# Kernel optimization log

Hardware: AMD Instinct MI355X
Metric: run time of the kernel (lower is better)

The kernel has to match this reference:

```python
import jax, jax.numpy as jnp
import numpy as np

N = 50000      # nodes
E = 800000     # edges (before self loops)
B = 64         # graphs in batch
D_IN, D_HID, D_LAT, N_CLS = 3, 128, 64, 2


def _gat_params(key, d_in, d_out, scale=0.1):
    k1, k2, k3 = jax.random.split(key, 3)
    return (jax.random.normal(k1, (d_in, d_out), jnp.float32) * scale,
            jax.random.normal(k2, (d_out,), jnp.float32) * scale,
            jax.random.normal(k3, (d_out,), jnp.float32) * scale,
            jnp.zeros((d_out,), jnp.float32))


def setup_inputs() -> dict:
    key = jax.random.key(0)
    ks = jax.random.split(key, 10)
    x = jax.random.normal(ks[0], (N, D_IN), jnp.float32)
    edge_index = jax.random.randint(ks[1], (2, E), 0, N, dtype=jnp.int64)
    batch = jnp.sort(jax.random.randint(ks[2], (N,), 0, B, dtype=jnp.int64))
    W1, a1s, a1d, b1 = _gat_params(ks[3], D_IN, D_HID)
    W2, a2s, a2d, b2 = _gat_params(ks[4], D_HID, D_LAT)
    W3, a3s, a3d, b3 = _gat_params(ks[5], D_LAT, D_HID)
    W4, a4s, a4d, b4 = _gat_params(ks[6], D_HID, D_IN)
    kc1, kc2 = jax.random.split(ks[7])
    Wc1 = jax.random.normal(kc1, (D_LAT, D_LAT // 2), jnp.float32) * 0.1
    bc1 = jnp.zeros((D_LAT // 2,), jnp.float32)
    Wc2 = jax.random.normal(kc2, (D_LAT // 2, N_CLS), jnp.float32) * 0.1
    bc2 = jnp.zeros((N_CLS,), jnp.float32)
    return dict(x=x, edge_index=edge_index, batch=batch,
                W1=W1, a1s=a1s, a1d=a1d, b1=b1,
                W2=W2, a2s=a2s, a2d=a2d, b2=b2,
                W3=W3, a3s=a3s, a3d=a3d, b3=b3,
                W4=W4, a4s=a4s, a4d=a4d, b4=b4,
                Wc1=Wc1, bc1=bc1, Wc2=Wc2, bc2=bc2)


def gat_conv(x, W, a_src, a_dst, bias, send, recv, n):
    # Single-head PyG GATConv: h = xW; e_ij = LeakyReLU(a_src.h_j + a_dst.h_i);
    # alpha = softmax over incoming edges of i; out_i = sum_j alpha_ij h_j + b
    h = x @ W                                   # [n, d_out]
    e = jax.nn.leaky_relu(jnp.take(h @ a_src, send) + jnp.take(h @ a_dst, recv), 0.2)
    m = jax.ops.segment_max(e, recv, num_segments=n)   # stable softmax per dst
    e = jnp.exp(e - m[recv])
    s = jax.ops.segment_sum(e, recv, num_segments=n)
    alpha = e / s[recv]                         # [E+N]
    out = jax.ops.segment_sum(alpha[:, None] * h[send], recv, num_segments=n)
    return out + bias


def reference(x, edge_index, batch,
              W1, a1s, a1d, b1, W2, a2s, a2d, b2,
              W3, a3s, a3d, b3, W4, a4s, a4d, b4,
              Wc1, bc1, Wc2, bc2):
    loop = jnp.arange(N, dtype=edge_index.dtype)
    send = jnp.concatenate([edge_index[0], loop])   # add_self_loops=True
    recv = jnp.concatenate([edge_index[1], loop])
    # encode (dropout inactive in eval)
    h = jax.nn.relu(gat_conv(x, W1, a1s, a1d, b1, send, recv, N))
    latent = gat_conv(h, W2, a2s, a2d, b2, send, recv, N)
    # decode
    h = jax.nn.relu(gat_conv(latent, W3, a3s, a3d, b3, send, recv, N))
    reconstructed = gat_conv(h, W4, a4s, a4d, b4, send, recv, N)
    # per-graph mean pooling (segment mean, replaces Python loop)
    cnt = jax.ops.segment_sum(jnp.ones((N,), latent.dtype), batch, num_segments=B)
    pooled = jax.ops.segment_sum(latent, batch, num_segments=B) / jnp.maximum(cnt, 1.0)[:, None]
    z = jax.nn.relu(pooled @ Wc1 + bc1)
    noise_pred = z @ Wc2 + bc2
    return reconstructed, latent, noise_pred
```

## Files before the change

kernel.cpp:

```cpp
#include <hip/hip_runtime.h>
#include <hip/hip_bf16.h>

typedef __hip_bfloat16 bf16;

#define N_NODES 50000
#define N_EDGES 800000
#define NB 64

#define NBUCK 256
#define BUCK_R ((N_NODES + NBUCK - 1) / NBUCK)
#define BUCK_CAP 4352
#define OVF_CAP 65536
#define NBLK1 256
#define CHUNK1 ((N_EDGES + NBLK1 - 1) / NBLK1)
#define NIT ((CHUNK1 + 255) / 256)

#define XN_BLKS ((N_NODES + 255) / 256)
#define PREP_BLKS (XN_BLKS + 20 + 1)

#define P_W1 0
#define P_A1S 384
#define P_A1D 512
#define P_B1 640
#define P_W2 768
#define P_A2S 8960
#define P_A2D 9024
#define P_B2 9088
#define P_W3 9152
#define P_A3S 17344
#define P_A3D 17472
#define P_B3 17600
#define P_W4 17728
#define P_A4S 18112
#define P_A4D 18115
#define P_B4 18118
#define P_WC1 18121
#define P_BC1 20169
#define P_WC2 20201
#define P_BC2 20265
#define P_W3S 20280
#define P_W3D 20344
#define P_TOTAL 20408

__device__ __forceinline__ float wave_sum(float v) {
#pragma unroll
    for (int o = 32; o >= 1; o >>= 1) v += __shfl_xor(v, o, 64);
    return v;
}

__device__ __forceinline__ unsigned int pk2(float a, float b) {
    bf16 x = __float2bfloat16(a);
    bf16 y = __float2bfloat16(b);
    unsigned short ux = *reinterpret_cast<unsigned short*>(&x);
    unsigned short uy = *reinterpret_cast<unsigned short*>(&y);
    return ((unsigned int)uy << 16) | ux;
}
__device__ __forceinline__ float bf_lo(unsigned int u) {
    unsigned int v = u << 16;
    return *reinterpret_cast<float*>(&v);
}
__device__ __forceinline__ float bf_hi(unsigned int u) {
    unsigned int v = u & 0xffff0000u;
    return *reinterpret_cast<float*>(&v);
}

__device__ __forceinline__ int ld_idx(const void* p, long long i, int is64) {
    return is64 ? (int)((const long long*)p)[i] : ((const int*)p)[i];
}
__device__ __forceinline__ float ldf(const void* p, int i, int isbf) {
    return isbf ? __bfloat162float(((const bf16*)p)[i]) : ((const float*)p)[i];
}
__device__ __forceinline__ void st_out(void* p, long long i, float v, int isbf) {
    if (isbf) ((bf16*)p)[i] = __float2bfloat16(v);
    else ((float*)p)[i] = v;
}

__device__ __forceinline__ float attn_p(float esv, float edi) {
    float v = esv + edi;
    float e = (v >= 0.f) ? v : 0.2f * v;
    return __expf(fminf(e, 60.f));
}

struct PTab {
    const void* src[20];
    int off[20];
    int n[20];
};

__global__ __launch_bounds__(256) void k_prep(
        const void* __restrict__ x, const void* __restrict__ eidx,
        const void* __restrict__ rW1, const void* __restrict__ rA1s,
        const void* __restrict__ rA1d, const void* __restrict__ rW3,
        const void* __restrict__ rA3s, const void* __restrict__ rA3d,
        PTab tab, float* __restrict__ pblock, float* __restrict__ x4,
        float* __restrict__ es, float* __restrict__ ed,
        int* __restrict__ gcur, int* __restrict__ ovf_cnt, int* __restrict__ flags) {
    __shared__ int scnt[2];
    __shared__ float sw[6];
    const int t = threadIdx.x;
    if (t < 2) scnt[t] = 0;
    __syncthreads();
    {
        const unsigned short* xr = (const unsigned short*)x;
        unsigned int hb = (xr[2 * t] >> 8) & 0x7F;
        if (hb >= 58 && hb <= 65) atomicAdd(&scnt[0], 1);
        if (t < 64) {
            const unsigned int* er = (const unsigned int*)eidx;
            if (er[2 * t + 1] == 0u) atomicAdd(&scnt[1], 1);
        }
    }
    __syncthreads();
    const int isbf = (scnt[0] >= 200) ? 1 : 0;
    const int is64 = (scnt[1] >= 60) ? 1 : 0;

    const int b = blockIdx.x;
    if (b < XN_BLKS) {
        if (t < 6) {
            int row = (t < 3) ? t : t - 3;
            const void* av = (t < 3) ? rA1s : rA1d;
            float s = 0.f;
            for (int k = 0; k < 128; k++)
                s = fmaf(ldf(rW1, row * 128 + k, isbf), ldf(av, k, isbf), s);
            sw[t] = s;
        }
        __syncthreads();
        int node = b * 256 + t;
        if (node < N_NODES) {
            float x0 = ldf(x, node * 3 + 0, isbf);
            float x1 = ldf(x, node * 3 + 1, isbf);
            float x2 = ldf(x, node * 3 + 2, isbf);
            float4 v = {x0, x1, x2, 0.f};
            *(float4*)&x4[node * 4] = v;
            es[node] = x0 * sw[0] + x1 * sw[1] + x2 * sw[2];
            ed[node] = x0 * sw[3] + x1 * sw[4] + x2 * sw[5];
        }
    } else if (b < XN_BLKS + 20) {
        int p = b - XN_BLKS;
        const void* s = tab.src[p];
        float* d = pblock + tab.off[p];
        int n = tab.n[p];
        for (int i = t; i < n; i += 256) d[i] = ldf(s, i, isbf);
    } else {
        if (t < NBUCK) gcur[t] = 0;
        if (t == 0) { *ovf_cnt = 0; flags[0] = isbf; flags[1] = is64; }
        if (t >= 64 && t < 128) {
            int k = t - 64;
            float s = 0.f, d = 0.f;
            for (int c = 0; c < 128; c++) {
                float wv = ldf(rW3, k * 128 + c, isbf);
                s = fmaf(wv, ldf(rA3s, c, isbf), s);
                d = fmaf(wv, ldf(rA3d, c, isbf), d);
            }
            pblock[P_W3S + k] = s;
            pblock[P_W3D + k] = d;
        }
    }
}

__global__ __launch_bounds__(256) void k_bucket(
        const void* __restrict__ eidx, const int* __restrict__ flags,
        int* __restrict__ gcur, unsigned int* __restrict__ stage,
        int* __restrict__ ovf_cnt, uint2* __restrict__ ovf) {
    __shared__ int hist[NBUCK];
    __shared__ int base[NBUCK];
    const int t = threadIdx.x;
    const int is64 = flags[1];
    const int e0 = blockIdx.x * CHUNK1;
    const int e1 = min(e0 + CHUNK1, N_EDGES);

    unsigned int ent[NIT];
    int bk[NIT];
    hist[t] = 0;
    __syncthreads();
#pragma unroll
    for (int it = 0; it < NIT; it++) {
        int e = e0 + t + it * 256;
        int b = -1;
        unsigned int en = 0;
        if (e < e1) {
            int r = ld_idx(eidx, (long long)N_EDGES + e, is64);
            int s = ld_idx(eidx, e, is64);
            b = r / BUCK_R;
            en = ((unsigned)(r - b * BUCK_R) << 16) | (unsigned)s;
            atomicAdd(&hist[b], 1);
        }
        ent[it] = en;
        bk[it] = b;
    }
    __syncthreads();
    int cnt = hist[t];
    base[t] = (cnt > 0) ? atomicAdd(&gcur[t], cnt) : 0;
    __syncthreads();
    hist[t] = 0;
    __syncthreads();
#pragma unroll
    for (int it = 0; it < NIT; it++) {
        int b = bk[it];
        if (b >= 0) {
            int l = atomicAdd(&hist[b], 1);
            int slot = base[b] + l;
            if (slot < BUCK_CAP) {
                stage[(size_t)b * BUCK_CAP + slot] = ent[it];
            } else {
                int oi = atomicAdd(ovf_cnt, 1);
                int r = b * BUCK_R + (int)(ent[it] >> 16);
                if (oi < OVF_CAP) ovf[oi] = make_uint2(ent[it] & 0xffffu, (unsigned)r);
            }
        }
    }
}

__global__ __launch_bounds__(256) void k_count2(
        const int* __restrict__ gcur, const unsigned int* __restrict__ stage,
        const int* __restrict__ ovf_cnt, const uint2* __restrict__ ovf,
        int* __restrict__ loff, int* __restrict__ bsum) {
    __shared__ int hist[256];
    __shared__ int ss[256];
    const int b = blockIdx.x;
    const int r0 = b * BUCK_R;
    const int nr = min(BUCK_R, N_NODES - r0);
    const int t = threadIdx.x;
    hist[t] = 0;
    __syncthreads();
    const int cnt = min(gcur[b], BUCK_CAP);
    const unsigned int* sb = stage + (size_t)b * BUCK_CAP;
    for (int i = t; i < cnt; i += 256) atomicAdd(&hist[sb[i] >> 16], 1);
    int oc = min(*ovf_cnt, OVF_CAP);
    for (int i = t; i < oc; i += 256) {
        int r = (int)ovf[i].y;
        if (r >= r0 && r < r0 + nr) atomicAdd(&hist[r - r0], 1);
    }
    __syncthreads();
    int v = (t < nr) ? hist[t] + 1 : 0;
    ss[t] = v;
    __syncthreads();
#pragma unroll
    for (int o = 1; o < 256; o <<= 1) {
        int add = (t >= o) ? ss[t - o] : 0;
        __syncthreads();
        ss[t] += add;
        __syncthreads();
    }
    if (t < nr) loff[r0 + t] = ss[t] - v;
    if (t == 255) bsum[b] = ss[255];
}

__global__ __launch_bounds__(256) void k_fill3(
        const int* __restrict__ gcur, const unsigned int* __restrict__ stage,
        const int* __restrict__ ovf_cnt, const uint2* __restrict__ ovf,
        const int* __restrict__ loff, const int* __restrict__ bsum,
        int* __restrict__ off, int* __restrict__ csr_send) {
    __shared__ int sbs[NBUCK];
    __shared__ int ss[NBUCK];
    __shared__ int sstart[BUCK_R];
    __shared__ int lcur[BUCK_R];
    const int b = blockIdx.x;
    const int t = threadIdx.x;
    int v = bsum[t];
    sbs[t] = v;
    ss[t] = v;
    __syncthreads();
#pragma unroll
    for (int o = 1; o < NBUCK; o <<= 1) {
        int add = (t >= o) ? ss[t - o] : 0;
        __syncthreads();
        ss[t] += add;
        __syncthreads();
    }
    const int bb = ss[b] - sbs[b];
    if (b == NBUCK - 1 && t == 0) off[N_NODES] = ss[NBUCK - 1];

    const int r0 = b * BUCK_R;
    const int nr = min(BUCK_R, N_NODES - r0);
    for (int i = t; i < nr; i += 256) {
        int st = bb + loff[r0 + i];
        sstart[i] = st;
        off[r0 + i] = st;
        lcur[i] = 1;
        csr_send[st] = r0 + i;
    }
    __syncthreads();
    const int cnt = min(gcur[b], BUCK_CAP);
    const unsigned int* sb = stage + (size_t)b * BUCK_CAP;
    for (int i = t; i < cnt; i += 256) {
        unsigned int e = sb[i];
        int rl = (int)(e >> 16);
        int l = atomicAdd(&lcur[rl], 1);
        csr_send[sstart[rl] + l] = (int)(e & 0xffffu);
    }
    int oc = min(*ovf_cnt, OVF_CAP);
    for (int i = t; i < oc; i += 256) {
        uint2 pr = ovf[i];
        int r = (int)pr.y;
        if (r >= r0 && r < r0 + nr) {
            int rl = r - r0;
            int l = atomicAdd(&lcur[rl], 1);
            csr_send[sstart[rl] + l] = (int)pr.x;
        }
    }
}

__global__ __launch_bounds__(256) void k_wsumx3(
        const float* __restrict__ x4, const float* __restrict__ es,
        const float* __restrict__ ed, const float* __restrict__ pb,
        const int* __restrict__ off, const int* __restrict__ csr_send,
        float* __restrict__ out) {
    int wid = threadIdx.x >> 6, lane = threadIdx.x & 63;
    int node = blockIdx.x * 4 + wid;
    if (node >= N_NODES) return;
    int start = off[node], end = off[node + 1];
    float edi = ed[node];
    float a0 = 0.f, a1 = 0.f, a2 = 0.f, sl = 0.f;
    for (int j = start + lane; j < end; j += 64) {
        int s = csr_send[j];
        float p = attn_p(es[s], edi);
        sl += p;
        float4 xv = *(const float4*)&x4[s * 4];
        a0 = fmaf(p, xv.x, a0);
        a1 = fmaf(p, xv.y, a1);
        a2 = fmaf(p, xv.z, a2);
    }
    float S = wave_sum(sl);
    a0 = wave_sum(a0);
    a1 = wave_sum(a1);
    a2 = wave_sum(a2);
    float inv = 1.f / S;
    a0 *= inv; a1 *= inv; a2 *= inv;
    const float* W1 = pb + P_W1;
    const float* b1 = pb + P_B1;
    int c0 = lane, c1 = lane + 64;
    float v0 = fmaf(a0, W1[c0], fmaf(a1, W1[128 + c0], fmaf(a2, W1[256 + c0], b1[c0])));
    float v1 = fmaf(a0, W1[c1], fmaf(a1, W1[128 + c1], fmaf(a2, W1[256 + c1], b1[c1])));
    out[(size_t)node * 128 + c0] = fmaxf(v0, 0.f);
    out[(size_t)node * 128 + c1] = fmaxf(v1, 0.f);
}

template <int DIN, int DINS, int DOUT, int MODE>
__global__ __launch_bounds__(256) void k_gemm(
        const float* __restrict__ in, const float* __restrict__ W,
        const float* __restrict__ as_, const float* __restrict__ ad_,
        const float* __restrict__ bias, void* __restrict__ hout,
        float* __restrict__ es, float* __restrict__ ed) {
    constexpr int KC = (DIN < 32) ? DIN : 32;
    constexpr int NCH = DIN / KC;
    constexpr int CG = DOUT / 8;
    constexpr int NT = (256 / CG) * 4;
    constexpr int NTP = NT + 4;

    __shared__ float sX[KC][NTP];
    __shared__ float sW[KC][DOUT];

    const int t = threadIdx.x;
    const int node0 = blockIdx.x * NT;
    const int nvalid = min(NT, N_NODES - node0);

    const int cg = t & (CG - 1);
    const int ng = t / CG;

    float acc[4][8] = {};

    for (int ch = 0; ch < NCH; ch++) {
        const int k0 = ch * KC;
        if (ch > 0) __syncthreads();
        for (int i = t; i < nvalid * KC; i += 256) {
            int n = i / KC, k = i - n * KC;
            sX[k][n] = in[(size_t)(node0 + n) * DINS + k0 + k];
        }
        for (int i = t; i < KC * DOUT; i += 256) {
            int k = i / DOUT, c = i - k * DOUT;
            sW[k][c] = W[(size_t)(k0 + k) * DOUT + c];
        }
        __syncthreads();

#pragma unroll 4
        for (int k = 0; k < KC; k++) {
            float4 xv = *(const float4*)&sX[k][ng * 4];
            float4 w0 = *(const float4*)&sW[k][cg * 8];
            float4 w1 = *(const float4*)&sW[k][cg * 8 + 4];
            float xs[4] = {xv.x, xv.y, xv.z, xv.w};
            float ws[8] = {w0.x, w0.y, w0.z, w0.w, w1.x, w1.y, w1.z, w1.w};
#pragma unroll
            for (int j = 0; j < 4; j++)
#pragma unroll
                for (int c = 0; c < 8; c++)
                    acc[j][c] = fmaf(xs[j], ws[c], acc[j][c]);
        }
    }

    if constexpr (MODE == 0) {
        float asv[8], adv[8];
#pragma unroll
        for (int c = 0; c < 8; c++) {
            asv[c] = as_[cg * 8 + c];
            adv[c] = ad_[cg * 8 + c];
        }
#pragma unroll
        for (int j = 0; j < 4; j++) {
            int n = ng * 4 + j;
            float e_s = 0.f, e_d = 0.f;
#pragma unroll
            for (int c = 0; c < 8; c++) {
                e_s = fmaf(acc[j][c], asv[c], e_s);
                e_d = fmaf(acc[j][c], adv[c], e_d);
            }
#pragma unroll
            for (int m = 1; m < CG; m <<= 1) {
                e_s += __shfl_xor(e_s, m, 64);
                e_d += __shfl_xor(e_d, m, 64);
            }
            if (n < nvalid) {
                if (cg == 0) {
                    es[node0 + n] = e_s;
                    ed[node0 + n] = e_d;
                }
                unsigned short* hb = (unsigned short*)hout;
                uint4 u;
                u.x = pk2(acc[j][0], acc[j][1]);
                u.y = pk2(acc[j][2], acc[j][3]);
                u.z = pk2(acc[j][4], acc[j][5]);
                u.w = pk2(acc[j][6], acc[j][7]);
                *(uint4*)&hb[(size_t)(node0 + n) * DOUT + cg * 8] = u;
            }
        }
    } else {
        const float* pbase = as_;
        const float* W4 = pbase + P_W4;
        float bv[8], w40[8], w41[8], w42[8];
#pragma unroll
        for (int c = 0; c < 8; c++) {
            bv[c] = bias[cg * 8 + c];
            int row = cg * 8 + c;
            w40[c] = W4[row * 3 + 0];
            w41[c] = W4[row * 3 + 1];
            w42[c] = W4[row * 3 + 2];
        }
        float a4s0 = pbase[P_A4S], a4s1 = pbase[P_A4S + 1], a4s2 = pbase[P_A4S + 2];
        float a4d0 = pbase[P_A4D], a4d1 = pbase[P_A4D + 1], a4d2 = pbase[P_A4D + 2];
        float* h3o = (float*)hout;
#pragma unroll
        for (int j = 0; j < 4; j++) {
            int n = ng * 4 + j;
            float h40 = 0.f, h41 = 0.f, h42 = 0.f;
#pragma unroll
            for (int c = 0; c < 8; c++) {
                float v = fmaxf(acc[j][c] + bv[c], 0.f);
                h40 = fmaf(v, w40[c], h40);
                h41 = fmaf(v, w41[c], h41);
                h42 = fmaf(v, w42[c], h42);
            }
#pragma unroll
            for (int m = 1; m < CG; m <<= 1) {
                h40 += __shfl_xor(h40, m, 64);
                h41 += __shfl_xor(h41, m, 64);
                h42 += __shfl_xor(h42, m, 64);
            }
            if (n < nvalid && cg == 0) {
                es[node0 + n] = h40 * a4s0 + h41 * a4s1 + h42 * a4s2;
                ed[node0 + n] = h40 * a4d0 + h41 * a4d1 + h42 * a4d2;
                float4 vv = {h40, h41, h42, 0.f};
                *(float4*)&h3o[(size_t)(node0 + n) * 4] = vv;
            }
        }
    }
}

__global__ __launch_bounds__(256) void k_wsum64f(
        const unsigned short* __restrict__ hb, const float* __restrict__ es,
        const float* __restrict__ ed, const float* __restrict__ pb,
        const int* __restrict__ off, const int* __restrict__ csr_send,
        float* __restrict__ out, unsigned short* __restrict__ lat16,
        float* __restrict__ es2, float* __restrict__ ed2,
        void* __restrict__ out_dev, long long out_off, const int* __restrict__ flags) {
    int wid = threadIdx.x >> 6, lane = threadIdx.x & 63;
    int node = blockIdx.x * 4 + wid;
    if (node >= N_NODES) return;
    int start = off[node], end = off[node + 1];
    float edi = ed[node];

    const int qd = lane >> 4;
    const int ql = lane & 15;
    float4 a0 = {0.f, 0.f, 0.f, 0.f}, a1 = {0.f, 0.f, 0.f, 0.f};
    float4 a2 = {0.f, 0.f, 0.f, 0.f}, a3 = {0.f, 0.f, 0.f, 0.f};
    float sl = 0.f;

    for (int base = start; base < end; base += 64) {
        int j = base + lane;
        bool valid = j < end;
        int src = valid ? csr_send[j] : 0;
        float p = valid ? attn_p(es[src], edi) : 0.f;
        sl += p;
        int cnt = min(64, end - base);
        int nq = (cnt + 3) >> 2;
        int j2 = 0;
        for (; j2 + 4 <= nq; j2 += 4) {
            int qA = 4 * j2 + qd;
            float pA = __shfl(p, qA, 64);      int sA = __shfl(src, qA, 64);
            float pB = __shfl(p, qA + 4, 64);  int sB = __shfl(src, qA + 4, 64);
            float pC = __shfl(p, qA + 8, 64);  int sC = __shfl(src, qA + 8, 64);
            float pD = __shfl(p, qA + 12, 64); int sD = __shfl(src, qA + 12, 64);
            uint2 uA = *((const uint2*)(hb + (size_t)sA * 64) + ql);
            uint2 uB = *((const uint2*)(hb + (size_t)sB * 64) + ql);
            uint2 uC = *((const uint2*)(hb + (size_t)sC * 64) + ql);
            uint2 uD = *((const uint2*)(hb + (size_t)sD * 64) + ql);
            a0.x = fmaf(pA, bf_lo(uA.x), a0.x); a0.y = fmaf(pA, bf_hi(uA.x), a0.y);
            a0.z = fmaf(pA, bf_lo(uA.y), a0.z); a0.w = fmaf(pA, bf_hi(uA.y), a0.w);
            a1.x = fmaf(pB, bf_lo(uB.x), a1.x); a1.y = fmaf(pB, bf_hi(uB.x), a1.y);
            a1.z = fmaf(pB, bf_lo(uB.y), a1.z); a1.w = fmaf(pB, bf_hi(uB.y), a1.w);
            a2.x = fmaf(pC, bf_lo(uC.x), a2.x); a2.y = fmaf(pC, bf_hi(uC.x), a2.y);
            a2.z = fmaf(pC, bf_lo(uC.y), a2.z); a2.w = fmaf(pC, bf_hi(uC.y), a2.w);
            a3.x = fmaf(pD, bf_lo(uD.x), a3.x); a3.y = fmaf(pD, bf_hi(uD.x), a3.y);
            a3.z = fmaf(pD, bf_lo(uD.y), a3.z); a3.w = fmaf(pD, bf_hi(uD.y), a3.w);
        }
        for (; j2 < nq; j2++) {
            int q = 4 * j2 + qd;
            float pq = __shfl(p, q, 64); int sq = __shfl(src, q, 64);
            uint2 u = *((const uint2*)(hb + (size_t)sq * 64) + ql);
            a0.x = fmaf(pq, bf_lo(u.x), a0.x); a0.y = fmaf(pq, bf_hi(u.x), a0.y);
            a0.z = fmaf(pq, bf_lo(u.y), a0.z); a0.w = fmaf(pq, bf_hi(u.y), a0.w);
        }
    }
    float S = wave_sum(sl);
    float inv = 1.f / S;
    float4 r;
    r.x = (a0.x + a1.x) + (a2.x + a3.x);
    r.y = (a0.y + a1.y) + (a2.y + a3.y);
    r.z = (a0.z + a1.z) + (a2.z + a3.z);
    r.w = (a0.w + a1.w) + (a2.w + a3.w);
    r.x += __shfl_xor(r.x, 16, 64); r.y += __shfl_xor(r.y, 16, 64);
    r.z += __shfl_xor(r.z, 16, 64); r.w += __shfl_xor(r.w, 16, 64);
    r.x += __shfl_xor(r.x, 32, 64); r.y += __shfl_xor(r.y, 32, 64);
    r.z += __shfl_xor(r.z, 32, 64); r.w += __shfl_xor(r.w, 32, 64);
    if (qd == 0) {
        float4 b = ((const float4*)(pb + P_B2))[ql];
        r.x = fmaf(r.x, inv, b.x); r.y = fmaf(r.y, inv, b.y);
        r.z = fmaf(r.z, inv, b.z); r.w = fmaf(r.w, inv, b.w);
        ((float4*)(out + (size_t)node * 64))[ql] = r;
        uint2 u = {pk2(r.x, r.y), pk2(r.z, r.w)};
        ((uint2*)(lat16 + (size_t)node * 64))[ql] = u;
        int isbf = flags[0];
        long long o4 = out_off + (long long)node * 64 + 4 * ql;
        st_out(out_dev, o4 + 0, r.x, isbf);
        st_out(out_dev, o4 + 1, r.y, isbf);
        st_out(out_dev, o4 + 2, r.z, isbf);
        st_out(out_dev, o4 + 3, r.w, isbf);
        const float* w3s = pb + P_W3S;
        const float* w3d = pb + P_W3D;
        float s3 = r.x * w3s[4 * ql] + r.y * w3s[4 * ql + 1] +
                   r.z * w3s[4 * ql + 2] + r.w * w3s[4 * ql + 3];
        float d3 = r.x * w3d[4 * ql] + r.y * w3d[4 * ql + 1] +
                   r.z * w3d[4 * ql + 2] + r.w * w3d[4 * ql + 3];
#pragma unroll
        for (int o = 8; o >= 1; o >>= 1) {
            s3 += __shfl_xor(s3, o, 64);
            d3 += __shfl_xor(d3, o, 64);
        }
        if (ql == 0) { es2[node] = s3; ed2[node] = d3; }
    }
}

__global__ __launch_bounds__(256) void k_wsumx64(
        const unsigned short* __restrict__ lat16, const float* __restrict__ es,
        const float* __restrict__ ed, const int* __restrict__ off,
        const int* __restrict__ csr_send, float* __restrict__ lagg) {
    int wid = threadIdx.x >> 6, lane = threadIdx.x & 63;
    int node = blockIdx.x * 4 + wid;
    if (node >= N_NODES) return;
    int start = off[node], end = off[node + 1];
    float edi = ed[node];

    const int qd = lane >> 4;
    const int ql = lane & 15;
    float4 a0 = {0.f, 0.f, 0.f, 0.f}, a1 = {0.f, 0.f, 0.f, 0.f};
    float4 a2 = {0.f, 0.f, 0.f, 0.f}, a3 = {0.f, 0.f, 0.f, 0.f};
    float sl = 0.f;

    for (int base = start; base < end; base += 64) {
        int j = base + lane;
        bool valid = j < end;
        int src = valid ? csr_send[j] : 0;
        float p = valid ? attn_p(es[src], edi) : 0.f;
        sl += p;
        int cnt = min(64, end - base);
        int nq = (cnt + 3) >> 2;
        int j2 = 0;
        for (; j2 + 4 <= nq; j2 += 4) {
            int qA = 4 * j2 + qd;
            float pA = __shfl(p, qA, 64);      int sA = __shfl(src, qA, 64);
            float pB = __shfl(p, qA + 4, 64);  int sB = __shfl(src, qA + 4, 64);
            float pC = __shfl(p, qA + 8, 64);  int sC = __shfl(src, qA + 8, 64);
            float pD = __shfl(p, qA + 12, 64); int sD = __shfl(src, qA + 12, 64);
            uint2 uA = *((const uint2*)(lat16 + (size_t)sA * 64) + ql);
            uint2 uB = *((const uint2*)(lat16 + (size_t)sB * 64) + ql);
            uint2 uC = *((const uint2*)(lat16 + (size_t)sC * 64) + ql);
            uint2 uD = *((const uint2*)(lat16 + (size_t)sD * 64) + ql);
            a0.x = fmaf(pA, bf_lo(uA.x), a0.x); a0.y = fmaf(pA, bf_hi(uA.x), a0.y);
            a0.z = fmaf(pA, bf_lo(uA.y), a0.z); a0.w = fmaf(pA, bf_hi(uA.y), a0.w);
            a1.x = fmaf(pB, bf_lo(uB.x), a1.x); a1.y = fmaf(pB, bf_hi(uB.x), a1.y);
            a1.z = fmaf(pB, bf_lo(uB.y), a1.z); a1.w = fmaf(pB, bf_hi(uB.y), a1.w);
            a2.x = fmaf(pC, bf_lo(uC.x), a2.x); a2.y = fmaf(pC, bf_hi(uC.x), a2.y);
            a2.z = fmaf(pC, bf_lo(uC.y), a2.z); a2.w = fmaf(pC, bf_hi(uC.y), a2.w);
            a3.x = fmaf(pD, bf_lo(uD.x), a3.x); a3.y = fmaf(pD, bf_hi(uD.x), a3.y);
            a3.z = fmaf(pD, bf_lo(uD.y), a3.z); a3.w = fmaf(pD, bf_hi(uD.y), a3.w);
        }
        for (; j2 < nq; j2++) {
            int q = 4 * j2 + qd;
            float pq = __shfl(p, q, 64); int sq = __shfl(src, q, 64);
            uint2 u = *((const uint2*)(lat16 + (size_t)sq * 64) + ql);
            a0.x = fmaf(pq, bf_lo(u.x), a0.x); a0.y = fmaf(pq, bf_hi(u.x), a0.y);
            a0.z = fmaf(pq, bf_lo(u.y), a0.z); a0.w = fmaf(pq, bf_hi(u.y), a0.w);
        }
    }
    float S = wave_sum(sl);
    float inv = 1.f / S;
    float4 r;
    r.x = (a0.x + a1.x) + (a2.x + a3.x);
    r.y = (a0.y + a1.y) + (a2.y + a3.y);
    r.z = (a0.z + a1.z) + (a2.z + a3.z);
    r.w = (a0.w + a1.w) + (a2.w + a3.w);
    r.x += __shfl_xor(r.x, 16, 64); r.y += __shfl_xor(r.y, 16, 64);
    r.z += __shfl_xor(r.z, 16, 64); r.w += __shfl_xor(r.w, 16, 64);
    r.x += __shfl_xor(r.x, 32, 64); r.y += __shfl_xor(r.y, 32, 64);
    r.z += __shfl_xor(r.z, 32, 64); r.w += __shfl_xor(r.w, 32, 64);
    if (qd == 0) {
        r.x *= inv; r.y *= inv; r.z *= inv; r.w *= inv;
        ((float4*)(lagg + (size_t)node * 64))[ql] = r;
    }
}

__global__ __launch_bounds__(256) void k_wsum3f(
        const float* __restrict__ h, const float* __restrict__ es,
        const float* __restrict__ ed, const float* __restrict__ bias,
        const int* __restrict__ off, const int* __restrict__ csr_send,
        void* __restrict__ out_dev, long long out_off, const int* __restrict__ flags) {
    int wid = threadIdx.x >> 6, lane = threadIdx.x & 63;
    int node = blockIdx.x * 4 + wid;
    if (node >= N_NODES) return;
    int start = off[node], end = off[node + 1];
    float edi = ed[node];

    float a0 = 0.f, a1 = 0.f, a2 = 0.f, sl = 0.f;
    for (int j = start + lane; j < end; j += 64) {
        int s = csr_send[j];
        float p = attn_p(es[s], edi);
        sl += p;
        float4 rv = *(const float4*)(h + (size_t)s * 4);
        a0 = fmaf(p, rv.x, a0);
        a1 = fmaf(p, rv.y, a1);
        a2 = fmaf(p, rv.z, a2);
    }
    float S = wave_sum(sl);
    a0 = wave_sum(a0);
    a1 = wave_sum(a1);
    a2 = wave_sum(a2);
    if (lane < 3) {
        float inv = 1.f / S;
        float v = fmaf((lane == 0 ? a0 : (lane == 1 ? a1 : a2)), inv, bias[lane]);
        st_out(out_dev, out_off + (long long)node * 3 + lane, v, flags[0]);
    }
}

#define POOL_W 16
__global__ void k_poolcls(const float* __restrict__ latent, const void* __restrict__ batch,
                          const int* __restrict__ flags, const float* __restrict__ pb,
                          void* __restrict__ out_dev, long long out_off) {
    int b = blockIdx.x;
    int lane = threadIdx.x & 63;
    int wave = threadIdx.x >> 6;
    int is64 = flags[1];
    int lo = 0, hi = N_NODES;
    while (lo < hi) { int mid = (lo + hi) >> 1; if (ld_idx(batch, mid, is64) < b) lo = mid + 1; else hi = mid; }
    int start = lo;
    lo = 0; hi = N_NODES;
    while (lo < hi) { int mid = (lo + hi) >> 1; if (ld_idx(batch, mid, is64) < b + 1) lo = mid + 1; else hi = mid; }
    int end = lo;
    float s = 0.f;
    for (int n = start + wave; n < end; n += POOL_W) s += latent[(size_t)n * 64 + lane];
    __shared__ float red[POOL_W][64];
    __shared__ float ps[64];
    red[wave][lane] = s;
    __syncthreads();
    if (wave == 0) {
        float t = s;
#pragma unroll
        for (int w2 = 1; w2 < POOL_W; w2++) t += red[w2][lane];
        float cnt = (float)(end - start);
        ps[lane] = t / fmaxf(cnt, 1.f);
    }
    __syncthreads();
    if (wave == 0 && lane < 32) {
        float z = pb[P_BC1 + lane];
        for (int c = 0; c < 64; c++) z = fmaf(ps[c], pb[P_WC1 + c * 32 + lane], z);
        z = fmaxf(z, 0.f);
        float p0 = z * pb[P_WC2 + lane * 2];
        float p1 = z * pb[P_WC2 + lane * 2 + 1];
#pragma unroll
        for (int o = 16; o >= 1; o >>= 1) {
            p0 += __shfl_xor(p0, o, 64);
            p1 += __shfl_xor(p1, o, 64);
        }
        if (lane == 0) {
            int isbf = flags[0];
            st_out(out_dev, out_off + b * 2 + 0, p0 + pb[P_BC2], isbf);
            st_out(out_dev, out_off + b * 2 + 1, p1 + pb[P_BC2 + 1], isbf);
        }
    }
}

extern "C" void kernel_launch(void* const* d_in, const int* in_sizes, int n_in,
                              void* d_out, int out_size, void* d_ws, size_t ws_size,
                              hipStream_t stream) {
    const void* x    = d_in[0];
    const void* eidx = d_in[1];
    const void* batch= d_in[2];

    char* w = (char*)d_ws;
    size_t o = 0;
    auto carve = [&](size_t bytes) { void* p = w + o; o = (o + bytes + 255) & ~(size_t)255; return p; };
    int* flags    = (int*)carve(8 * sizeof(int));
    int* off      = (int*)carve((N_NODES + 1) * sizeof(int));
    int* loff     = (int*)carve(N_NODES * sizeof(int));
    int* bsum     = (int*)carve(NBUCK * sizeof(int));
    int* gcur     = (int*)carve(NBUCK * sizeof(int));
    int* ovf_cnt  = (int*)carve(sizeof(int));
    int* csr_send = (int*)carve((size_t)(N_EDGES + N_NODES) * sizeof(int));
    unsigned int* stage = (unsigned int*)carve((size_t)NBUCK * BUCK_CAP * sizeof(unsigned int));
    uint2* ovf    = (uint2*)carve((size_t)OVF_CAP * sizeof(uint2));
    float* pblock = (float*)carve(P_TOTAL * sizeof(float));
    float* x4     = (float*)carve((size_t)N_NODES * 4 * sizeof(float));
    float* buf0   = (float*)carve((size_t)N_NODES * 128 * sizeof(float));
    unsigned short* hb = (unsigned short*)carve((size_t)N_NODES * 64 * sizeof(unsigned short));
    unsigned short* lat16 = (unsigned short*)carve((size_t)N_NODES * 64 * sizeof(unsigned short));
    float* lagg   = (float*)carve((size_t)N_NODES * 64 * sizeof(float));
    float* h3     = (float*)carve((size_t)N_NODES * 4 * sizeof(float));
    float* es     = (float*)carve(N_NODES * sizeof(float));
    float* ed     = (float*)carve(N_NODES * sizeof(float));
    float* es2    = (float*)carve(N_NODES * sizeof(float));
    float* ed2    = (float*)carve(N_NODES * sizeof(float));

    int gW = N_NODES / 4;

    PTab tab;
    const int pn[20]  = {384,128,128,128, 8192,64,64,64, 8192,128,128,128, 384,3,3,3, 2048,32,64,2};
    const int pof[20] = {P_W1,P_A1S,P_A1D,P_B1, P_W2,P_A2S,P_A2D,P_B2, P_W3,P_A3S,P_A3D,P_B3,
                         P_W4,P_A4S,P_A4D,P_B4, P_WC1,P_BC1,P_WC2,P_BC2};
    for (int i = 0; i < 20; i++) { tab.src[i] = d_in[3 + i]; tab.off[i] = pof[i]; tab.n[i] = pn[i]; }
    k_prep<<<PREP_BLKS, 256, 0, stream>>>(x, eidx, d_in[3], d_in[4], d_in[5],
                                          d_in[11], d_in[12], d_in[13],
                                          tab, pblock, x4, es, ed, gcur, ovf_cnt, flags);

    k_bucket<<<NBLK1, 256, 0, stream>>>(eidx, flags, gcur, stage, ovf_cnt, ovf);
    k_count2<<<NBUCK, 256, 0, stream>>>(gcur, stage, ovf_cnt, ovf, loff, bsum);
    k_fill3<<<NBUCK, 256, 0, stream>>>(gcur, stage, ovf_cnt, ovf, loff, bsum, off, csr_send);

    const long long OFF_RECON = 0, OFF_LATENT = 150000, OFF_NOISE = 3350000;

    int g128 = (N_NODES + 127) / 128;
    int g64  = (N_NODES + 63) / 64;

    k_wsumx3<<<gW, 256, 0, stream>>>(x4, es, ed, pblock, off, csr_send, buf0);

    k_gemm<128, 128, 64, 0><<<g128, 256, 0, stream>>>(buf0, pblock + P_W2, pblock + P_A2S,
                                                      pblock + P_A2D, pblock, hb, es, ed);
    k_wsum64f<<<gW, 256, 0, stream>>>(hb, es, ed, pblock, off, csr_send,
                                      buf0, lat16, es2, ed2, d_out, OFF_LATENT, flags);

    k_poolcls<<<NB, POOL_W * 64, 0, stream>>>(buf0, batch, flags, pblock, d_out, OFF_NOISE);

    k_wsumx64<<<gW, 256, 0, stream>>>(lat16, es2, ed2, off, csr_send, lagg);
    k_gemm<64, 64, 128, 3><<<g64, 256, 0, stream>>>(lagg, pblock + P_W3, pblock, pblock,
                                                    pblock + P_B3, h3, es, ed);

    k_wsum3f<<<gW, 256, 0, stream>>>(h3, es, ed, pblock + P_B4, off, csr_send,
                                     d_out, OFF_RECON, flags);
}
```

Measured before the change: 216.5 us.

## Merge CSR count and fill kernels; use 16-lane groups per node for narrow aggregations

Folds the per-bucket histogram and scan kernel into the fill kernel. Each block now recomputes the global bucket totals itself, from gcur, an overflow histogram and the row counts, which removes one launch and the loff/bsum round trip. The 3-wide aggregation kernels (layer 1 and layer 4) now give each node 16 lanes instead of a full 64-lane wave. With about 17 edges per node, this cuts idle lanes and the cost of reductions. The layer-1 output is written as float4 vectors. The cost is that every fill block scans the overflow list twice and does redundant scans.

```diff
diff --git a/kernel.cpp b/kernel.cpp
--- a/kernel.cpp
+++ b/kernel.cpp
@@ -47,6 +47,11 @@
     for (int o = 32; o >= 1; o >>= 1) v += __shfl_xor(v, o, 64);
     return v;
 }
+__device__ __forceinline__ float g16_sum(float v) {
+#pragma unroll
+    for (int o = 8; o >= 1; o >>= 1) v += __shfl_xor(v, o, 64);
+    return v;
+}
 
 __device__ __forceinline__ unsigned int pk2(float a, float b) {
     bf16 x = __float2bfloat16(a);
@@ -210,54 +215,26 @@
     }
 }
 
-__global__ __launch_bounds__(256) void k_count2(
+__global__ __launch_bounds__(256) void k_fillc(
         const int* __restrict__ gcur, const unsigned int* __restrict__ stage,
         const int* __restrict__ ovf_cnt, const uint2* __restrict__ ovf,
-        int* __restrict__ loff, int* __restrict__ bsum) {
-    __shared__ int hist[256];
-    __shared__ int ss[256];
-    const int b = blockIdx.x;
-    const int r0 = b * BUCK_R;
-    const int nr = min(BUCK_R, N_NODES - r0);
-    const int t = threadIdx.x;
-    hist[t] = 0;
-    __syncthreads();
-    const int cnt = min(gcur[b], BUCK_CAP);
-    const unsigned int* sb = stage + (size_t)b * BUCK_CAP;
-    for (int i = t; i < cnt; i += 256) atomicAdd(&hist[sb[i] >> 16], 1);
-    int oc = min(*ovf_cnt, OVF_CAP);
-    for (int i = t; i < oc; i += 256) {
-        int r = (int)ovf[i].y;
-        if (r >= r0 && r < r0 + nr) atomicAdd(&hist[r - r0], 1);
-    }
-    __syncthreads();
-    int v = (t < nr) ? hist[t] + 1 : 0;
-    ss[t] = v;
-    __syncthreads();
-#pragma unroll
-    for (int o = 1; o < 256; o <<= 1) {
-        int add = (t >= o) ? ss[t - o] : 0;
-        __syncthreads();
-        ss[t] += add;
-        __syncthreads();
-    }
-    if (t < nr) loff[r0 + t] = ss[t] - v;
-    if (t == 255) bsum[b] = ss[255];
-}
-
-__global__ __launch_bounds__(256) void k_fill3(
-        const int* __restrict__ gcur, const unsigned int* __restrict__ stage,
-        const int* __restrict__ ovf_cnt, const uint2* __restrict__ ovf,
-        const int* __restrict__ loff, const int* __restrict__ bsum,
         int* __restrict__ off, int* __restrict__ csr_send) {
-    __shared__ int sbs[NBUCK];
+    __shared__ int ovh[NBUCK];
     __shared__ int ss[NBUCK];
     __shared__ int sstart[BUCK_R];
     __shared__ int lcur[BUCK_R];
     const int b = blockIdx.x;
     const int t = threadIdx.x;
-    int v = bsum[t];
-    sbs[t] = v;
+
+    ovh[t] = 0;
+    __syncthreads();
+    const int oc = min(*ovf_cnt, OVF_CAP);
+    for (int i = t; i < oc; i += 256) atomicAdd(&ovh[(int)ovf[i].y / BUCK_R], 1);
+    __syncthreads();
+
+    int nrb = N_NODES - t * BUCK_R;
+    nrb = (nrb < 0) ? 0 : ((nrb > BUCK_R) ? BUCK_R : nrb);
+    int v = min(gcur[t], BUCK_CAP) + ovh[t] + nrb;
     ss[t] = v;
     __syncthreads();
 #pragma unroll
@@ -267,28 +244,50 @@
         ss[t] += add;
         __syncthreads();
     }
-    const int bb = ss[b] - sbs[b];
-    if (b == NBUCK - 1 && t == 0) off[N_NODES] = ss[NBUCK - 1];
+    const int total_all = ss[NBUCK - 1];
+    int nrb_b = N_NODES - b * BUCK_R;
+    nrb_b = (nrb_b < 0) ? 0 : ((nrb_b > BUCK_R) ? BUCK_R : nrb_b);
+    const int vb = min(gcur[b], BUCK_CAP) + ovh[b] + nrb_b;
+    const int bstart = ss[b] - vb;
+    if (b == NBUCK - 1 && t == 0) off[N_NODES] = total_all;
+    __syncthreads();
 
     const int r0 = b * BUCK_R;
-    const int nr = min(BUCK_R, N_NODES - r0);
-    for (int i = t; i < nr; i += 256) {
-        int st = bb + loff[r0 + i];
-        sstart[i] = st;
-        off[r0 + i] = st;
-        lcur[i] = 1;
-        csr_send[st] = r0 + i;
-    }
+    const int nr = nrb_b;
+    ovh[t] = 0;
     __syncthreads();
     const int cnt = min(gcur[b], BUCK_CAP);
     const unsigned int* sb = stage + (size_t)b * BUCK_CAP;
+    for (int i = t; i < cnt; i += 256) atomicAdd(&ovh[sb[i] >> 16], 1);
+    for (int i = t; i < oc; i += 256) {
+        int r = (int)ovf[i].y;
+        if (r >= r0 && r < r0 + nr) atomicAdd(&ovh[r - r0], 1);
+    }
+    __syncthreads();
+    int vv = (t < nr) ? ovh[t] + 1 : 0;
+    ss[t] = vv;
+    __syncthreads();
+#pragma unroll
+    for (int o = 1; o < NBUCK; o <<= 1) {
+        int add = (t >= o) ? ss[t - o] : 0;
+        __syncthreads();
+        ss[t] += add;
+        __syncthreads();
+    }
+    if (t < nr) {
+        int st = bstart + ss[t] - vv;
+        sstart[t] = st;
+        off[r0 + t] = st;
+        lcur[t] = 1;
+        csr_send[st] = r0 + t;
+    }
+    __syncthreads();
     for (int i = t; i < cnt; i += 256) {
         unsigned int e = sb[i];
         int rl = (int)(e >> 16);
         int l = atomicAdd(&lcur[rl], 1);
         csr_send[sstart[rl] + l] = (int)(e & 0xffffu);
     }
-    int oc = min(*ovf_cnt, OVF_CAP);
     for (int i = t; i < oc; i += 256) {
         uint2 pr = ovf[i];
         int r = (int)pr.y;
@@ -305,13 +304,13 @@
         const float* __restrict__ ed, const float* __restrict__ pb,
         const int* __restrict__ off, const int* __restrict__ csr_send,
         float* __restrict__ out) {
-    int wid = threadIdx.x >> 6, lane = threadIdx.x & 63;
-    int node = blockIdx.x * 4 + wid;
+    int node = blockIdx.x * 16 + (threadIdx.x >> 4);
+    int l16 = threadIdx.x & 15;
     if (node >= N_NODES) return;
     int start = off[node], end = off[node + 1];
     float edi = ed[node];
     float a0 = 0.f, a1 = 0.f, a2 = 0.f, sl = 0.f;
-    for (int j = start + lane; j < end; j += 64) {
+    for (int j = start + l16; j < end; j += 16) {
         int s = csr_send[j];
         float p = attn_p(es[s], edi);
         sl += p;
@@ -320,19 +319,26 @@
         a1 = fmaf(p, xv.y, a1);
         a2 = fmaf(p, xv.z, a2);
     }
-    float S = wave_sum(sl);
-    a0 = wave_sum(a0);
-    a1 = wave_sum(a1);
-    a2 = wave_sum(a2);
+    float S = g16_sum(sl);
+    a0 = g16_sum(a0);
+    a1 = g16_sum(a1);
+    a2 = g16_sum(a2);
     float inv = 1.f / S;
     a0 *= inv; a1 *= inv; a2 *= inv;
     const float* W1 = pb + P_W1;
     const float* b1 = pb + P_B1;
-    int c0 = lane, c1 = lane + 64;
-    float v0 = fmaf(a0, W1[c0], fmaf(a1, W1[128 + c0], fmaf(a2, W1[256 + c0], b1[c0])));
-    float v1 = fmaf(a0, W1[c1], fmaf(a1, W1[128 + c1], fmaf(a2, W1[256 + c1], b1[c1])));
-    out[(size_t)node * 128 + c0] = fmaxf(v0, 0.f);
-    out[(size_t)node * 128 + c1] = fmaxf(v1, 0.f);
+    int c = l16 * 8;
+    float r[8];
+#pragma unroll
+    for (int k = 0; k < 8; k++) {
+        int cc = c + k;
+        float v = fmaf(a0, W1[cc], fmaf(a1, W1[128 + cc], fmaf(a2, W1[256 + cc], b1[cc])));
+        r[k] = fmaxf(v, 0.f);
+    }
+    float4 v0 = {r[0], r[1], r[2], r[3]};
+    float4 v1 = {r[4], r[5], r[6], r[7]};
+    *(float4*)&out[(size_t)node * 128 + c] = v0;
+    *(float4*)&out[(size_t)node * 128 + c + 4] = v1;
 }
 
 template <int DIN, int DINS, int DOUT, int MODE>
@@ -632,14 +638,14 @@
         const float* __restrict__ ed, const float* __restrict__ bias,
         const int* __restrict__ off, const int* __restrict__ csr_send,
         void* __restrict__ out_dev, long long out_off, const int* __restrict__ flags) {
-    int wid = threadIdx.x >> 6, lane = threadIdx.x & 63;
-    int node = blockIdx.x * 4 + wid;
+    int node = blockIdx.x * 16 + (threadIdx.x >> 4);
+    int l16 = threadIdx.x & 15;
     if (node >= N_NODES) return;
     int start = off[node], end = off[node + 1];
     float edi = ed[node];
 
     float a0 = 0.f, a1 = 0.f, a2 = 0.f, sl = 0.f;
-    for (int j = start + lane; j < end; j += 64) {
+    for (int j = start + l16; j < end; j += 16) {
         int s = csr_send[j];
         float p = attn_p(es[s], edi);
         sl += p;
@@ -648,14 +654,14 @@
         a1 = fmaf(p, rv.y, a1);
         a2 = fmaf(p, rv.z, a2);
     }
-    float S = wave_sum(sl);
-    a0 = wave_sum(a0);
-    a1 = wave_sum(a1);
-    a2 = wave_sum(a2);
-    if (lane < 3) {
+    float S = g16_sum(sl);
+    a0 = g16_sum(a0);
+    a1 = g16_sum(a1);
+    a2 = g16_sum(a2);
+    if (l16 < 3) {
         float inv = 1.f / S;
-        float v = fmaf((lane == 0 ? a0 : (lane == 1 ? a1 : a2)), inv, bias[lane]);
-        st_out(out_dev, out_off + (long long)node * 3 + lane, v, flags[0]);
+        float v = fmaf((l16 == 0 ? a0 : (l16 == 1 ? a1 : a2)), inv, bias[l16]);
+        st_out(out_dev, out_off + (long long)node * 3 + l16, v, flags[0]);
     }
 }
 
@@ -718,8 +724,6 @@
     auto carve = [&](size_t bytes) { void* p = w + o; o = (o + bytes + 255) & ~(size_t)255; return p; };
     int* flags    = (int*)carve(8 * sizeof(int));
     int* off      = (int*)carve((N_NODES + 1) * sizeof(int));
-    int* loff     = (int*)carve(N_NODES * sizeof(int));
-    int* bsum     = (int*)carve(NBUCK * sizeof(int));
     int* gcur     = (int*)carve(NBUCK * sizeof(int));
     int* ovf_cnt  = (int*)carve(sizeof(int));
     int* csr_send = (int*)carve((size_t)(N_EDGES + N_NODES) * sizeof(int));
@@ -738,6 +742,7 @@
     float* ed2    = (float*)carve(N_NODES * sizeof(float));
 
     int gW = N_NODES / 4;
+    int g16 = (N_NODES + 15) / 16;
 
     PTab tab;
     const int pn[20]  = {384,128,128,128, 8192,64,64,64, 8192,128,128,128, 384,3,3,3, 2048,32,64,2};
@@ -749,15 +754,14 @@
                                           tab, pblock, x4, es, ed, gcur, ovf_cnt, flags);
 
     k_bucket<<<NBLK1, 256, 0, stream>>>(eidx, flags, gcur, stage, ovf_cnt, ovf);
-    k_count2<<<NBUCK, 256, 0, stream>>>(gcur, stage, ovf_cnt, ovf, loff, bsum);
-    k_fill3<<<NBUCK, 256, 0, stream>>>(gcur, stage, ovf_cnt, ovf, loff, bsum, off, csr_send);
+    k_fillc<<<NBUCK, 256, 0, stream>>>(gcur, stage, ovf_cnt, ovf, off, csr_send);
 
     const long long OFF_RECON = 0, OFF_LATENT = 150000, OFF_NOISE = 3350000;
 
     int g128 = (N_NODES + 127) / 128;
     int g64  = (N_NODES + 63) / 64;
 
-    k_wsumx3<<<gW, 256, 0, stream>>>(x4, es, ed, pblock, off, csr_send, buf0);
+    k_wsumx3<<<g16, 256, 0, stream>>>(x4, es, ed, pblock, off, csr_send, buf0);
 
     k_gemm<128, 128, 64, 0><<<g128, 256, 0, stream>>>(buf0, pblock + P_W2, pblock + P_A2S,
                                                       pblock + P_A2D, pblock, hb, es, ed);
@@ -770,6 +774,6 @@
     k_gemm<64, 64, 128, 3><<<g64, 256, 0, stream>>>(lagg, pblock + P_W3, pblock, pblock,
                                                     pblock + P_B3, h3, es, ed);
 
-    k_wsum3f<<<gW, 256, 0, stream>>>(h3, es, ed, pblock + P_B4, off, csr_send,
-                                     d_out, OFF_RECON, flags);
-}
+    k_wsum3f<<<g16, 256, 0, stream>>>(h3, es, ed, pblock + P_B4, off, csr_send,
+                                      d_out, OFF_RECON, flags);
+}
```

New measurement: 204.9 us. 1.06x faster.
